# Performance work log

Hardware: AMD Instinct MI355X
Metric: run time of the kernel (lower is better)

## Reference

```python
import jax, jax.numpy as jnp
import numpy as np

# ---- constants matching init_kwargs ----
NUM_STEPS = 25
NEW_AMP = 2.0
ENC_THRESHOLD = 0.5   # encoder spike threshold
BETA = 0.95           # LIF leak
LIF_THRESHOLD = 1.0   # snntorch Leaky default threshold
FIL_LEN = 50
FIL_STD = 5.0


def _gaussian_window(M, std):
    n = np.arange(M, dtype=np.float32) - (M - 1) / 2.0
    return np.exp(-0.5 * (n / std) ** 2).astype(np.float32)


def setup_inputs() -> dict:
    key = jax.random.key(0)
    k1, k2, k3 = jax.random.split(key, 3)
    B, L, H, C = 131072, 187, 50, 5
    x = jax.random.normal(k1, (B, L), dtype=jnp.float32)
    filt = jnp.asarray(_gaussian_window(FIL_LEN, FIL_STD))
    W1 = jax.random.normal(k2, (H, L), dtype=jnp.float32) / np.sqrt(L)
    W2 = jax.random.normal(k3, (C, H), dtype=jnp.float32) / np.sqrt(H)
    return {"x": x, "filt": filt, "W1": W1, "W2": W2}


def _encoder(x, filt):
    # Gaussian smoothing (conv1d, SAME padding), amplify, threshold -> spikes
    B, L = x.shape
    K = filt.shape[0]
    y = jax.lax.conv_general_dilated(
        x[:, None, :], filt[None, None, :],
        window_strides=(1,), padding=[((K - 1) // 2, K // 2)],
        dimension_numbers=("NCH", "OIH", "NCH"))[:, 0, :]
    y = y * NEW_AMP
    return (y > ENC_THRESHOLD).astype(x.dtype)


def reference(x, filt, W1, W2):
    spikes = _encoder(x, filt)                 # [B, L], identical every step
    cur1 = spikes @ W1.T                       # [B, 50], constant over steps
    B = x.shape[0]
    mem1 = jnp.zeros((B, W1.shape[0]), x.dtype)
    mem2 = jnp.zeros((B, W2.shape[0]), x.dtype)

    def step(carry, _):
        m1, m2 = carry
        m1 = BETA * m1 + cur1
        spk1 = (m1 > LIF_THRESHOLD).astype(m1.dtype)
        m1 = m1 - spk1 * LIF_THRESHOLD         # reset-by-subtraction
        cur2 = spk1 @ W2.T
        m2 = BETA * m2 + cur2
        spk2 = (m2 > LIF_THRESHOLD).astype(m2.dtype)
        m2 = m2 - spk2 * LIF_THRESHOLD
        return (m1, m2), spk2

    (_, _), spk_rec = jax.lax.scan(step, (mem1, mem2), None, length=NUM_STEPS)
    spike_count = spikes.sum() * NUM_STEPS     # encoder.count_spike()
    return spk_rec, spike_count
```

## Files before the change

### kernel.cpp

```cpp
#include <hip/hip_runtime.h>


typedef float    f32x4 __attribute__((ext_vector_type(4)));
typedef short    s16x8 __attribute__((ext_vector_type(8)));

constexpr int L = 187;
constexpr int H = 50;
constexpr int NST = 25;
constexpr float BETA = 0.95f;
constexpr float YTH  = 0.25f;

constexpr int TTA_SH = 12 * 6 * 64 * 8;
constexpr int W1A_SH = 4 * 6 * 64 * 8;
constexpr int W2A_SH = 2 * 64 * 8;
constexpr int NPART  = 4096;

__device__ inline unsigned short f2bf(float f) {
    union { float f; unsigned u; } v; v.f = f;
    return (unsigned short)((v.u + 0x7FFFu + ((v.u >> 16) & 1u)) >> 16);
}

__global__ void __launch_bounds__(256) prep_frags(
    const float* __restrict__ filt, const float* __restrict__ W1,
    const float* __restrict__ W2,
    unsigned short* __restrict__ TtA, unsigned short* __restrict__ W1A,
    unsigned short* __restrict__ W2A)
{
    int i = blockIdx.x * 256 + threadIdx.x;
    if (i < TTA_SH) {
        int jj = i & 7, lane = (i >> 3) & 63, kt = (i >> 9) % 6, nt = i / (512 * 6);
        int lm = lane & 15, lk = lane >> 4;
        int l = 16 * nt + lm;
        int k = 32 * kt + 8 * lk + jj;
        int d = k - l + 24;
        unsigned short v = 0;
        if (l < L && k < L && d >= 0 && d < 50) v = f2bf(filt[d]);
        TtA[i] = v;
    } else if (i < TTA_SH + W1A_SH) {
        int i2 = i - TTA_SH;
        int jj = i2 & 7, lane = (i2 >> 3) & 63, kt = (i2 >> 9) % 6, mt = i2 / (512 * 6);
        int lm = lane & 15, lk = lane >> 4;
        int h = 16 * mt + lm;
        int l = 4 * lk + (jj & 3) + 16 * (2 * kt + (jj >> 2));
        unsigned short v = 0;
        if (h < H && l < L) v = f2bf(W1[h * L + l]);
        W1A[i2] = v;
    } else {
        int i3 = i - TTA_SH - W1A_SH;
        int jj = i3 & 7, lane = (i3 >> 3) & 63, kt = i3 >> 9;
        int lm = lane & 15, lk = lane >> 4;
        int h = 4 * lk + (jj & 3) + 16 * (2 * kt + (jj >> 2));
        unsigned short v = 0;
        if (lm < 5 && h < H) v = f2bf(W2[lm * H + h]);
        W2A[i3] = v;
    }
}

__global__ void __launch_bounds__(256, 4) snn_fused(
    const float* __restrict__ x,
    const unsigned short* __restrict__ TtA,
    const unsigned short* __restrict__ W1A,
    const unsigned short* __restrict__ W2A,
    float* __restrict__ out, unsigned int* __restrict__ part, int B)
{
    __shared__ unsigned int csh[4];

    const int tid = threadIdx.x;
    const int wid = tid >> 6, lane = tid & 63;
    const int lm = lane & 15, lk = lane >> 4;
    const int row = blockIdx.x * 64 + wid * 16 + lm;

    s16x8 xB[6];
    {
        const float* __restrict__ xr = x + (size_t)row * L;
        #pragma unroll
        for (int kt = 0; kt < 6; ++kt) {
            const int k0 = 32 * kt + 8 * lk;
            s16x8 v;
            if (k0 + 8 <= L) {
                float t[8];
                __builtin_memcpy(t, xr + k0, 32);
                #pragma unroll
                for (int jj = 0; jj < 8; ++jj) v[jj] = (short)f2bf(t[jj]);
            } else {
                #pragma unroll
                for (int jj = 0; jj < 8; ++jj) {
                    int k = k0 + jj;
                    v[jj] = (short)f2bf((k < L) ? xr[k] : 0.f);
                }
            }
            xB[kt] = v;
        }
    }

    int scnt = 0;
    s16x8 spkB[6];
    {
        constexpr int lo[6] = {0, 0, 1, 2, 3, 4};
        constexpr int hi[6] = {1, 2, 3, 4, 5, 5};
        #pragma unroll
        for (int p = 0; p < 6; ++p) {
            f32x4 y0 = (f32x4){0, 0, 0, 0}, y1 = (f32x4){0, 0, 0, 0};
            #pragma unroll
            for (int kt = 0; kt < 6; ++kt) {
                if (kt >= lo[p] && kt <= hi[p]) {
                    s16x8 a0 = *(const s16x8*)(TtA + ((size_t)((2 * p    ) * 6 + kt) * 64 + lane) * 8);
                    s16x8 a1 = *(const s16x8*)(TtA + ((size_t)((2 * p + 1) * 6 + kt) * 64 + lane) * 8);
                    y0 = __builtin_amdgcn_mfma_f32_16x16x32_bf16(a0, xB[kt], y0, 0, 0, 0);
                    y1 = __builtin_amdgcn_mfma_f32_16x16x32_bf16(a1, xB[kt], y1, 0, 0, 0);
                }
            }
            union { unsigned w[4]; s16x8 v; } pk;
            #pragma unroll
            for (int w = 0; w < 4; ++w) {
                float va = (w < 2) ? y0[2 * w]     : y1[2 * (w - 2)];
                float vb = (w < 2) ? y0[2 * w + 1] : y1[2 * (w - 2) + 1];
                bool s0 = va > YTH, s1 = vb > YTH;
                scnt += (int)s0 + (int)s1;
                pk.w[w] = (s0 ? 0x3F80u : 0u) | (s1 ? 0x3F800000u : 0u);
            }
            spkB[p] = pk.v;
        }
    }
    #pragma unroll
    for (int off = 32; off; off >>= 1) scnt += __shfl_down(scnt, off);
    if (lane == 0) csh[wid] = (unsigned)scnt;
    __syncthreads();
    if (tid == 0) part[blockIdx.x] = csh[0] + csh[1] + csh[2] + csh[3];

    f32x4 cu[4];
    #pragma unroll
    for (int mt = 0; mt < 4; ++mt) cu[mt] = (f32x4){0, 0, 0, 0};
    #pragma unroll
    for (int mt = 0; mt < 4; ++mt)
        #pragma unroll
        for (int kt = 0; kt < 6; ++kt) {
            s16x8 a = *(const s16x8*)(W1A + ((size_t)(mt * 6 + kt) * 64 + lane) * 8);
            cu[mt] = __builtin_amdgcn_mfma_f32_16x16x32_bf16(a, spkB[kt], cu[mt], 0, 0, 0);
        }

    s16x8 w2a[2];
    #pragma unroll
    for (int kt = 0; kt < 2; ++kt)
        w2a[kt] = *(const s16x8*)(W2A + ((size_t)kt * 64 + lane) * 8);

    f32x4 m1[4];
    #pragma unroll
    for (int mt = 0; mt < 4; ++mt) m1[mt] = (f32x4){0, 0, 0, 0};
    f32x4 m2 = (f32x4){0, 0, 0, 0};

    float* __restrict__ po = out + (size_t)row * 5;
    const size_t step = (size_t)B * 5;

    #pragma unroll 1
    for (int t = 0; t < NST; ++t) {
        s16x8 s1b[2];
        #pragma unroll
        for (int kt = 0; kt < 2; ++kt) {
            union { unsigned w[4]; s16x8 v; } pk;
            #pragma unroll
            for (int w = 0; w < 4; ++w) {
                const int jj0 = 2 * w, jj1 = 2 * w + 1;
                const int mt0 = 2 * kt + (jj0 >> 2), j0 = jj0 & 3;
                const int mt1 = 2 * kt + (jj1 >> 2), j1 = jj1 & 3;
                float ma = fmaf(BETA, m1[mt0][j0], cu[mt0][j0]);
                float mb = fmaf(BETA, m1[mt1][j1], cu[mt1][j1]);
                bool sa = ma > 1.f, sb = mb > 1.f;
                m1[mt0][j0] = sa ? ma - 1.f : ma;
                m1[mt1][j1] = sb ? mb - 1.f : mb;
                pk.w[w] = (sa ? 0x3F80u : 0u) | (sb ? 0x3F800000u : 0u);
            }
            s1b[kt] = pk.v;
        }
        f32x4 c2 = (f32x4){0, 0, 0, 0};
        c2 = __builtin_amdgcn_mfma_f32_16x16x32_bf16(w2a[0], s1b[0], c2, 0, 0, 0);
        c2 = __builtin_amdgcn_mfma_f32_16x16x32_bf16(w2a[1], s1b[1], c2, 0, 0, 0);
        f32x4 sv;
        #pragma unroll
        for (int j = 0; j < 4; ++j) {
            float m = fmaf(BETA, m2[j], c2[j]);
            bool s = m > 1.f;
            m2[j] = s ? m - 1.f : m;
            sv[j] = s ? 1.f : 0.f;
        }
        float* __restrict__ pt = po + (size_t)t * step;
        if (lk == 0) {
            __builtin_memcpy(pt, &sv, 16);
        } else if (lk == 1) {
            pt[4] = sv[0];
        }
    }
}

__global__ void __launch_bounds__(256) finalize_count(
    const unsigned int* __restrict__ part, int n,
    float* __restrict__ out, size_t off)
{
    __shared__ unsigned int sh[4];
    unsigned int s = 0;
    for (int i = threadIdx.x; i < n; i += 256) s += part[i];
    #pragma unroll
    for (int o = 32; o; o >>= 1) s += __shfl_down(s, o);
    if ((threadIdx.x & 63) == 0) sh[threadIdx.x >> 6] = s;
    __syncthreads();
    if (threadIdx.x == 0) {
        unsigned int t = sh[0] + sh[1] + sh[2] + sh[3];
        out[off] = (float)((double)t * 25.0);
    }
}

__global__ void __launch_bounds__(256) snn_fallback(
    const float* __restrict__ x, const float* __restrict__ filt,
    const float* __restrict__ W1, const float* __restrict__ W2,
    float* __restrict__ out, unsigned int* __restrict__ part, int B)
{
    __shared__ unsigned int csh[4];
    const int row = blockIdx.x * 256 + threadIdx.x;
    const bool valid = row < B;
    const int rr = valid ? row : (B - 1);
    const float* __restrict__ xr = x + (size_t)rr * L;
    float w[64], cur1[H];
    #pragma unroll
    for (int h = 0; h < H; ++h) cur1[h] = 0.f;
    int cntv = 0;
    #pragma unroll
    for (int i = 0; i < 64; ++i) w[i] = (i >= 24) ? xr[i - 24] : 0.f;
    #pragma unroll 1
    for (int s = 0; s < 12; ++s) {
        const int l0 = s * 15;
        #pragma unroll
        for (int j = 0; j < 15; ++j) {
            const int l = l0 + j;
            float yv = 0.f;
            #pragma unroll
            for (int k = 0; k < 50; ++k) yv = fmaf(w[j + k], filt[k], yv);
            const bool sb = yv > YTH;
            cntv += sb;
            const float sp = sb ? 1.f : 0.f;
            #pragma unroll
            for (int h = 0; h < H; ++h) cur1[h] = fmaf(sp, W1[h * L + l], cur1[h]);
        }
        #pragma unroll
        for (int i = 0; i < 49; ++i) w[i] = w[i + 15];
        #pragma unroll
        for (int d = 0; d < 15; ++d) {
            const int g = l0 + 40 + d;
            w[49 + d] = (g < L) ? xr[g] : 0.f;
        }
    }
    #pragma unroll
    for (int j = 0; j < 7; ++j) {
        const int l = 180 + j;
        float yv = 0.f;
        #pragma unroll
        for (int k = 0; k < 50; ++k) yv = fmaf(w[j + k], filt[k], yv);
        const bool sb = yv > YTH;
        cntv += sb;
        const float sp = sb ? 1.f : 0.f;
        #pragma unroll
        for (int h = 0; h < H; ++h) cur1[h] = fmaf(sp, W1[h * L + l], cur1[h]);
    }
    int wc = valid ? cntv : 0;
    #pragma unroll
    for (int off = 32; off; off >>= 1) wc += __shfl_down(wc, off);
    if ((threadIdx.x & 63) == 0) csh[threadIdx.x >> 6] = (unsigned)wc;
    __syncthreads();
    if (threadIdx.x == 0) part[blockIdx.x] = csh[0] + csh[1] + csh[2] + csh[3];
    float m1[H], m2[5];
    #pragma unroll
    for (int h = 0; h < H; ++h) m1[h] = 0.f;
    #pragma unroll
    for (int c = 0; c < 5; ++c) m2[c] = 0.f;
    #pragma unroll 1
    for (int t = 0; t < NST; ++t) {
        float c2[5] = {0, 0, 0, 0, 0};
        #pragma unroll
        for (int h = 0; h < H; ++h) {
            float m = fmaf(BETA, m1[h], cur1[h]);
            const float sp = (m > 1.f) ? 1.f : 0.f;
            m1[h] = m - sp;
            #pragma unroll
            for (int c = 0; c < 5; ++c) c2[c] = fmaf(sp, W2[c * H + h], c2[c]);
        }
        float* __restrict__ ot = out + ((size_t)t * B + rr) * 5;
        #pragma unroll
        for (int c = 0; c < 5; ++c) {
            float m = fmaf(BETA, m2[c], c2[c]);
            const float s2 = (m > 1.f) ? 1.f : 0.f;
            m2[c] = m - s2;
            if (valid) ot[c] = s2;
        }
    }
}

extern "C" void kernel_launch(void* const* d_in, const int* in_sizes, int n_in,
                              void* d_out, int out_size, void* d_ws, size_t ws_size,
                              hipStream_t stream)
{
    const float* x    = (const float*)d_in[0];
    const float* filt = (const float*)d_in[1];
    const float* W1   = (const float*)d_in[2];
    const float* W2   = (const float*)d_in[3];
    float* out        = (float*)d_out;
    const int B       = in_sizes[0] / L;

    unsigned int* part  = (unsigned int*)d_ws;
    unsigned short* TtA = (unsigned short*)((char*)d_ws + NPART * 4);
    unsigned short* W1A = TtA + TTA_SH;
    unsigned short* W2A = W1A + W1A_SH;
    const size_t need = (size_t)NPART * 4 + (size_t)(TTA_SH + W1A_SH + W2A_SH) * 2;

    if (ws_size >= need && (B % 64) == 0 && B / 64 <= NPART) {
        const int total = TTA_SH + W1A_SH + W2A_SH;
        prep_frags<<<(total + 255) / 256, 256, 0, stream>>>(filt, W1, W2, TtA, W1A, W2A);
        snn_fused<<<B / 64, 256, 0, stream>>>(x, TtA, W1A, W2A, out, part, B);
        finalize_count<<<1, 256, 0, stream>>>(part, B / 64, out, (size_t)NST * B * 5);
    } else {
        snn_fallback<<<(B + 255) / 256, 256, 0, stream>>>(x, filt, W1, W2, out, part, B);
        finalize_count<<<1, 256, 0, stream>>>(part, (B + 255) / 256, out, (size_t)NST * B * 5);
    }
}
```

Baseline: 63.65 us.

## Stage compact Toeplitz filter table and weight fragments in LDS

Replaces the precomputed banded Toeplitz fragment array with a compact shifted-filter table of 8 rows, indexed on the fly from the diagonal offset. The table, W1 and W2 fragments are copied into shared memory at block start, so MFMA operands come from LDS instead of repeated global/L2 loads. It also masks padded rows out of the spike count in the last tile. The cost is about 30 KB of LDS per block, which may limit occupancy, plus a block-wide barrier before compute.

```diff
diff --git a/kernel.cpp b/kernel.cpp
--- a/kernel.cpp
+++ b/kernel.cpp
@@ -10,7 +10,8 @@
 constexpr float BETA = 0.95f;
 constexpr float YTH  = 0.25f;
 
-constexpr int TTA_SH = 12 * 6 * 64 * 8;
+constexpr int FT_STR = 264;
+constexpr int FT_SH  = 8 * FT_STR;
 constexpr int W1A_SH = 4 * 6 * 64 * 8;
 constexpr int W2A_SH = 2 * 64 * 8;
 constexpr int NPART  = 4096;
@@ -22,53 +23,60 @@
 
 __global__ void __launch_bounds__(256) prep_frags(
     const float* __restrict__ filt, const float* __restrict__ W1,
-    const float* __restrict__ W2,
-    unsigned short* __restrict__ TtA, unsigned short* __restrict__ W1A,
-    unsigned short* __restrict__ W2A)
+    const float* __restrict__ W2, unsigned short* __restrict__ frags)
 {
     int i = blockIdx.x * 256 + threadIdx.x;
-    if (i < TTA_SH) {
-        int jj = i & 7, lane = (i >> 3) & 63, kt = (i >> 9) % 6, nt = i / (512 * 6);
-        int lm = lane & 15, lk = lane >> 4;
-        int l = 16 * nt + lm;
-        int k = 32 * kt + 8 * lk + jj;
-        int d = k - l + 24;
-        unsigned short v = 0;
-        if (l < L && k < L && d >= 0 && d < 50) v = f2bf(filt[d]);
-        TtA[i] = v;
-    } else if (i < TTA_SH + W1A_SH) {
-        int i2 = i - TTA_SH;
+    if (i < FT_SH) {
+        int r = i / FT_STR, m = i - r * FT_STR;
+        int idx = m + r - 48;
+        frags[i] = (idx >= 0 && idx < 50) ? f2bf(filt[idx]) : (unsigned short)0;
+    } else if (i < FT_SH + W1A_SH) {
+        int i2 = i - FT_SH;
         int jj = i2 & 7, lane = (i2 >> 3) & 63, kt = (i2 >> 9) % 6, mt = i2 / (512 * 6);
         int lm = lane & 15, lk = lane >> 4;
         int h = 16 * mt + lm;
         int l = 4 * lk + (jj & 3) + 16 * (2 * kt + (jj >> 2));
         unsigned short v = 0;
         if (h < H && l < L) v = f2bf(W1[h * L + l]);
-        W1A[i2] = v;
-    } else {
-        int i3 = i - TTA_SH - W1A_SH;
+        frags[i] = v;
+    } else if (i < FT_SH + W1A_SH + W2A_SH) {
+        int i3 = i - FT_SH - W1A_SH;
         int jj = i3 & 7, lane = (i3 >> 3) & 63, kt = i3 >> 9;
         int lm = lane & 15, lk = lane >> 4;
         int h = 4 * lk + (jj & 3) + 16 * (2 * kt + (jj >> 2));
         unsigned short v = 0;
         if (lm < 5 && h < H) v = f2bf(W2[lm * H + h]);
-        W2A[i3] = v;
+        frags[i] = v;
     }
 }
 
 __global__ void __launch_bounds__(256, 4) snn_fused(
     const float* __restrict__ x,
-    const unsigned short* __restrict__ TtA,
-    const unsigned short* __restrict__ W1A,
-    const unsigned short* __restrict__ W2A,
+    const unsigned short* __restrict__ frags,
     float* __restrict__ out, unsigned int* __restrict__ part, int B)
 {
+    __shared__ __align__(16) unsigned short ftabL[FT_SH];
+    __shared__ __align__(16) unsigned short W1L[W1A_SH];
+    __shared__ __align__(16) unsigned short W2L[W2A_SH];
     __shared__ unsigned int csh[4];
 
     const int tid = threadIdx.x;
     const int wid = tid >> 6, lane = tid & 63;
     const int lm = lane & 15, lk = lane >> 4;
     const int row = blockIdx.x * 64 + wid * 16 + lm;
+
+    {
+        const uint4* g = (const uint4*)frags;
+        uint4* sF = (uint4*)ftabL;
+        uint4* s1 = (uint4*)W1L;
+        uint4* s2 = (uint4*)W2L;
+        #pragma unroll 2
+        for (int i = tid; i < 264; i += 256) sF[i] = g[i];
+        #pragma unroll
+        for (int i = tid; i < 1536; i += 256) s1[i] = g[264 + i];
+        if (tid < 128) s2[tid] = g[264 + 1536 + tid];
+    }
+    __syncthreads();
 
     s16x8 xB[6];
     {
@@ -93,6 +101,7 @@
         }
     }
 
+    const int dl = 8 * lk - lm + 72;
     int scnt = 0;
     s16x8 spkB[6];
     {
@@ -104,8 +113,10 @@
             #pragma unroll
             for (int kt = 0; kt < 6; ++kt) {
                 if (kt >= lo[p] && kt <= hi[p]) {
-                    s16x8 a0 = *(const s16x8*)(TtA + ((size_t)((2 * p    ) * 6 + kt) * 64 + lane) * 8);
-                    s16x8 a1 = *(const s16x8*)(TtA + ((size_t)((2 * p + 1) * 6 + kt) * 64 + lane) * 8);
+                    const int D0a = dl + 32 * kt - 32 * p;
+                    const int D0b = D0a - 16;
+                    s16x8 a0 = *(const s16x8*)&ftabL[(D0a & 7) * FT_STR + (D0a & ~7)];
+                    s16x8 a1 = *(const s16x8*)&ftabL[(D0b & 7) * FT_STR + (D0b & ~7)];
                     y0 = __builtin_amdgcn_mfma_f32_16x16x32_bf16(a0, xB[kt], y0, 0, 0, 0);
                     y1 = __builtin_amdgcn_mfma_f32_16x16x32_bf16(a1, xB[kt], y1, 0, 0, 0);
                 }
@@ -116,7 +127,12 @@
                 float va = (w < 2) ? y0[2 * w]     : y1[2 * (w - 2)];
                 float vb = (w < 2) ? y0[2 * w + 1] : y1[2 * (w - 2) + 1];
                 bool s0 = va > YTH, s1 = vb > YTH;
-                scnt += (int)s0 + (int)s1;
+                bool ok0 = true, ok1 = true;
+                if (p == 5 && w >= 2) {
+                    ok0 = (4 * lk + 2 * (w - 2))     < 11;
+                    ok1 = (4 * lk + 2 * (w - 2) + 1) < 11;
+                }
+                scnt += (int)(s0 & ok0) + (int)(s1 & ok1);
                 pk.w[w] = (s0 ? 0x3F80u : 0u) | (s1 ? 0x3F800000u : 0u);
             }
             spkB[p] = pk.v;
@@ -135,14 +151,14 @@
     for (int mt = 0; mt < 4; ++mt)
         #pragma unroll
         for (int kt = 0; kt < 6; ++kt) {
-            s16x8 a = *(const s16x8*)(W1A + ((size_t)(mt * 6 + kt) * 64 + lane) * 8);
+            s16x8 a = *(const s16x8*)&W1L[((mt * 6 + kt) * 64 + lane) * 8];
             cu[mt] = __builtin_amdgcn_mfma_f32_16x16x32_bf16(a, spkB[kt], cu[mt], 0, 0, 0);
         }
 
     s16x8 w2a[2];
     #pragma unroll
     for (int kt = 0; kt < 2; ++kt)
-        w2a[kt] = *(const s16x8*)(W2A + ((size_t)kt * 64 + lane) * 8);
+        w2a[kt] = *(const s16x8*)&W2L[(kt * 64 + lane) * 8];
 
     f32x4 m1[4];
     #pragma unroll
@@ -304,16 +320,14 @@
     float* out        = (float*)d_out;
     const int B       = in_sizes[0] / L;
 
-    unsigned int* part  = (unsigned int*)d_ws;
-    unsigned short* TtA = (unsigned short*)((char*)d_ws + NPART * 4);
-    unsigned short* W1A = TtA + TTA_SH;
-    unsigned short* W2A = W1A + W1A_SH;
-    const size_t need = (size_t)NPART * 4 + (size_t)(TTA_SH + W1A_SH + W2A_SH) * 2;
+    unsigned int* part    = (unsigned int*)d_ws;
+    unsigned short* frags = (unsigned short*)((char*)d_ws + NPART * 4);
+    const int total_sh    = FT_SH + W1A_SH + W2A_SH;
+    const size_t need     = (size_t)NPART * 4 + (size_t)total_sh * 2;
 
     if (ws_size >= need && (B % 64) == 0 && B / 64 <= NPART) {
-        const int total = TTA_SH + W1A_SH + W2A_SH;
-        prep_frags<<<(total + 255) / 256, 256, 0, stream>>>(filt, W1, W2, TtA, W1A, W2A);
-        snn_fused<<<B / 64, 256, 0, stream>>>(x, TtA, W1A, W2A, out, part, B);
+        prep_frags<<<(total_sh + 255) / 256, 256, 0, stream>>>(filt, W1, W2, frags);
+        snn_fused<<<B / 64, 256, 0, stream>>>(x, frags, out, part, B);
         finalize_count<<<1, 256, 0, stream>>>(part, B / 64, out, (size_t)NST * B * 5);
     } else {
         snn_fallback<<<(B + 255) / 256, 256, 0, stream>>>(x, filt, W1, W2, out, part, B);
```

Measured after the change: 60.46 us. 1.05x faster.
